# Kernel tuning notes

Measured on AMD Instinct MI355X. Metric: run time of the kernel, lower is better.

The kernel has to match this reference:

```python
import jax, jax.numpy as jnp
import numpy as np
from jax import lax

B, DIM, H, W = 32, 64, 1, 8192
HEADS = 8
EPS_LN = 1e-5
EPS_NORM = 1e-12


def setup_inputs() -> dict:
    key = jax.random.key(0)
    ks = jax.random.split(key, 20)
    g = lambda i, shape, s=0.05: jax.random.normal(ks[i], shape, jnp.float32) * s
    return dict(
        x=jax.random.normal(ks[0], (B, DIM, H, W), jnp.float32),
        qkv_w=g(1, (3 * DIM, DIM)), qkv_b=g(2, (3 * DIM,)),
        dw_w=g(3, (3 * DIM, 1, 3, 3)), dw_b=g(4, (3 * DIM,)),
        proj_w=g(5, (DIM, DIM)), proj_b=g(6, (DIM,)),
        temperature=jnp.ones((HEADS, 1, 1), jnp.float32),
        sp_w=g(7, (DIM,)), sp_b=g(8, (1,)),
        up_w=g(9, (3,)), up_b=g(10, (3,)),
        c2_w=g(11, (1, 1, 2)), c2_b=g(11, (1,)), ln2_w=jnp.ones((W,), jnp.float32), ln2_b=jnp.zeros((W,), jnp.float32),
        c4_w=g(12, (1, 1, 4)), c4_b=g(13, (1,)), ln4_w=jnp.ones((W,), jnp.float32), ln4_b=jnp.zeros((W,), jnp.float32),
        c6_w=g(14, (1, 1, 6)), c6_b=g(15, (1,)), ln6_w=jnp.ones((W,), jnp.float32), ln6_b=jnp.zeros((W,), jnp.float32),
        mp_w=g(16, (DIM,)), mp_b=g(17, (DIM,)),
    )


def _mtl(xs, cw, cb, lw, lb):
    """Multiscale_Temporal_Layer: conv1d 'same' -> LayerNorm(W) -> ELU -> mean pool. xs: (b,1,w)."""
    k = cw.shape[-1]
    tot = k - 1
    lo = tot // 2  # torch 'same': extra pad goes to the right
    y = lax.conv_general_dilated(xs, cw, (1,), [(lo, tot - lo)],
                                 dimension_numbers=('NCH', 'OIH', 'NCH'))
    y = y + cb[None, :, None]
    mu = jnp.mean(y, -1, keepdims=True)
    var = jnp.mean((y - mu) ** 2, -1, keepdims=True)
    y = (y - mu) / jnp.sqrt(var + EPS_LN) * lw + lb
    y = jax.nn.elu(y)
    return jnp.mean(y, -1, keepdims=True)  # (b,1,1)


def _forward(x, qkv_w, qkv_b, dw_w, dw_b, proj_w, proj_b, temperature,
             sp_w, sp_b, up_w, up_b,
             c2_w, c2_b, ln2_w, ln2_b,
             c4_w, c4_b, ln4_w, ln4_b,
             c6_w, c6_b, ln6_w, ln6_b,
             mp_w, mp_b):
    b, c, h, w = x.shape
    hd = c // HEADS  # per-head channel dim
    # 1x1 conv qkv, then depthwise 3x3 conv
    qkv = jnp.einsum('oc,bchw->bohw', qkv_w, x) + qkv_b[None, :, None, None]
    qkv = lax.conv_general_dilated(qkv, dw_w, (1, 1), [(1, 1), (1, 1)],
                                   dimension_numbers=('NCHW', 'OIHW', 'NCHW'),
                                   feature_group_count=3 * c)
    qkv = qkv + dw_b[None, :, None, None]
    q, k, v = jnp.split(qkv, 3, axis=1)
    # Multiscale_Temporal_Attention on v: v is (b,c,1,w)
    xseq = (jnp.einsum('c,bcw->bw', sp_w, v[:, :, 0, :]) + sp_b)[:, None, :]  # (b,1,w)
    up = up_w[None, :, None] * xseq + up_b[None, :, None]  # (b,3,w)
    xx, yy, zz = up[:, 0:1], up[:, 1:2], up[:, 2:3]
    mout = (_mtl(xx, c2_w, c2_b, ln2_w, ln2_b) * xx
            + _mtl(yy, c4_w, c4_b, ln4_w, ln4_b) * yy
            + _mtl(zz, c6_w, c6_b, ln6_w, ln6_b) * zz)  # (b,1,w)
    v = mp_w[None, :, None] * mout + mp_b[None, :, None]  # (b,c,w) via 1x1 conv broadcast
    # channel (transposed) attention over n = h*w tokens
    n = h * w
    q = q.reshape(b, HEADS, hd, n)
    k = k.reshape(b, HEADS, hd, n)
    v = v.reshape(b, HEADS, hd, n)
    q = q / jnp.maximum(jnp.linalg.norm(q, axis=-1, keepdims=True), EPS_NORM)
    k = k / jnp.maximum(jnp.linalg.norm(k, axis=-1, keepdims=True), EPS_NORM)
    attn = jnp.einsum('bhcn,bhdn->bhcd', q, k) * temperature  # (b,heads,hd,hd)
    attn = jax.nn.softmax(attn, axis=-1)
    out = jnp.einsum('bhcd,bhdn->bhcn', attn, v).reshape(b, c, h, w)
    out = jnp.einsum('oc,bchw->bohw', proj_w, out) + proj_b[None, :, None, None]
    return out  # dropouts are identity in eval mode


def reference(x, qkv_w, qkv_b, dw_w, dw_b, proj_w, proj_b, temperature,
              sp_w, sp_b, up_w, up_b,
              c2_w, c2_b, ln2_w, ln2_b,
              c4_w, c4_b, ln4_w, ln4_b,
              c6_w, c6_b, ln6_w, ln6_b,
              mp_w, mp_b):
    return _forward(x, qkv_w, qkv_b, dw_w, dw_b, proj_w, proj_b, temperature,
                    sp_w, sp_b, up_w, up_b,
                    c2_w, c2_b, ln2_w, ln2_b,
                    c4_w, c4_b, ln4_w, ln4_b,
                    c6_w, c6_b, ln6_w, ln6_b,
                    mp_w, mp_b)
```

## Files before the change

kernel.cpp:

```cpp
#include <hip/hip_runtime.h>
#include <hip/hip_bf16.h>
#include <math.h>

#define Wd 8192
#define Bd 32
#define Ttile 64

#define OFF_G    0
#define OFF_H    192
#define OFF_BASE 195
#define OFF_XSEQ 256
#define OFF_PART (256 + Bd*Wd)
#define OFF_S    (OFF_PART + Bd*128*640)
#define OFF_M    (OFF_S + Bd*640)
#define OFF_E    (OFF_M + 96)
#define OFF_F    (OFF_E + Bd*64)
#define OFF_FRAG (OFF_F + Bd*64)

typedef __attribute__((ext_vector_type(8))) short bf16x8;
typedef __attribute__((ext_vector_type(4))) float f32x4;

__device__ __forceinline__ unsigned short f2bf(float v) {
    return __builtin_bit_cast(unsigned short, __float2bfloat16(v));
}
__device__ __forceinline__ float bf2f(unsigned short h) {
    return __builtin_bit_cast(float, (unsigned)h << 16);
}
__device__ __forceinline__ void split2(float v0, float v1, unsigned& hw, unsigned& lw) {
    unsigned short h0 = f2bf(v0), h1 = f2bf(v1);
    unsigned short l0 = f2bf(v0 - bf2f(h0)), l1 = f2bf(v1 - bf2f(h1));
    hw = (unsigned)h0 | ((unsigned)h1 << 16);
    lw = (unsigned)l0 | ((unsigned)l1 << 16);
}
__device__ __forceinline__ unsigned pk2(float v0, float v1) {
    return (unsigned)f2bf(v0) | ((unsigned)f2bf(v1) << 16);
}

__global__ __launch_bounds__(256) void k0_setup(const float* __restrict__ qkv_w,
                         const float* __restrict__ qkv_b,
                         const float* __restrict__ dw_w, const float* __restrict__ dw_b,
                         const float* __restrict__ sp_w, const float* __restrict__ sp_b,
                         float* __restrict__ ws)
{
    int tid = threadIdx.x;
    if (tid < 192) {
        int j = tid >> 6, ch = tid & 63;
        float acc = 0.f;
        for (int c = 0; c < 64; c++)
            acc += sp_w[c] * dw_w[(128+c)*9 + 3 + j] * qkv_w[(128+c)*64 + ch];
        ws[OFF_G + j*64 + ch] = acc;
    } else if (tid < 195) {
        int j = tid - 192;
        float h = 0.f;
        for (int c = 0; c < 64; c++)
            h += sp_w[c] * dw_w[(128+c)*9 + 3 + j] * qkv_b[128+c];
        ws[OFF_H + j] = h;
    } else if (tid == 195) {
        float base = sp_b[0];
        for (int c = 0; c < 64; c++) base += sp_w[c] * dw_b[128+c];
        ws[OFF_BASE] = base;
    }
    __syncthreads();
    for (int it = tid; it < 36*64; it += 256) {
        int lane = it & 63;
        int cidx = it >> 6;
        int ver = cidx / 18;
        int rem = cidx - ver*18;
        int nt = rem >> 1, kb = rem & 1;
        int row = nt*16 + (lane & 15);
        int ks  = kb*32 + (lane >> 4)*8;
        unsigned short u[8];
        #pragma unroll
        for (int e = 0; e < 8; e++) {
            int k = ks + e;
            float v = 0.f;
            if (row < 128)      v = qkv_w[row*64 + k];
            else if (row < 131) v = ws[OFF_G + (row-128)*64 + k];
            unsigned short h = f2bf(v);
            if (ver == 0) u[e] = h;
            else          u[e] = f2bf(v - bf2f(h));
        }
        unsigned* dst = (unsigned*)(ws + OFF_FRAG) + (ver*1152 + (nt*2+kb)*64 + lane)*4;
        dst[0] = (unsigned)u[0] | ((unsigned)u[1] << 16);
        dst[1] = (unsigned)u[2] | ((unsigned)u[3] << 16);
        dst[2] = (unsigned)u[4] | ((unsigned)u[5] << 16);
        dst[3] = (unsigned)u[6] | ((unsigned)u[7] << 16);
    }
}

#define XT_HI 0
#define XT_LO 10752
#define QKH   21504
#define ZLDS  37888
#define SMEM_BYTES (37888 + 1024)

__global__ __launch_bounds__(256, 4) void k1_main(const float* __restrict__ x,
    const float* __restrict__ qkv_b, const float* __restrict__ dw_w,
    const float* __restrict__ dw_b, float* __restrict__ ws)
{
    __shared__ __align__(16) unsigned char smem[SMEM_BYTES];
    const int tid = threadIdx.x, lane = tid & 63, wv = tid >> 6;
    const int g = lane >> 4, lr = lane & 15;
    const int tile = blockIdx.x, b = blockIdx.y;
    const int w0 = tile * Ttile;
    const float* xb = x + (size_t)b * 64 * Wd;
    const bool safe = (tile != 0) && (tile != 127);

    for (int i = tid; i < 672; i += 256) {
        int j = i >> 5, chp = i & 31;
        int pos0 = w0 - 4 + 4*j;
        float4 a, c;
        if (safe || (unsigned)pos0 < (unsigned)Wd) {
            a = *(const float4*)(xb + (size_t)(2*chp)*Wd + pos0);
            c = *(const float4*)(xb + (size_t)(2*chp+1)*Wd + pos0);
        } else {
            a = (float4){0,0,0,0}; c = (float4){0,0,0,0};
        }
        #pragma unroll
        for (int e = 0; e < 4; e++) {
            int row = 4*j + e;
            float va = ((const float*)&a)[e], vc = ((const float*)&c)[e];
            unsigned hw, lw;
            split2(va, vc, hw, lw);
            int boff = row*128 + ((((chp>>2) ^ (row & 7)) << 4) | ((chp & 3) << 2));
            *(unsigned*)(smem + XT_HI + boff) = hw;
            *(unsigned*)(smem + XT_LO + boff) = lw;
        }
    }
    __syncthreads();

    f32x4 acc[3][5];
    #pragma unroll
    for (int i = 0; i < 3; i++)
        #pragma unroll
        for (int m = 0; m < 5; m++) acc[i][m] = (f32x4){0.f,0.f,0.f,0.f};
    const uint4* fragbase = (const uint4*)(ws + OFF_FRAG);

    #pragma unroll
    for (int kb = 0; kb < 2; kb++) {
        bf16x8 axh[5], axl[5];
        #pragma unroll
        for (int mt = 0; mt < 5; mt++) {
            int row = mt*16 + lr + 3;
            int gran = (kb*4 + g) ^ (row & 7);
            axh[mt] = *(const bf16x8*)(smem + XT_HI + row*128 + gran*16);
            axl[mt] = *(const bf16x8*)(smem + XT_LO + row*128 + gran*16);
        }
        #pragma unroll
        for (int nti = 0; nti < 3; nti++) {
            if (nti < 2 || wv == 0) {
                int nt = (nti == 2) ? 8 : (wv + nti*4);
                bf16x8 bh = __builtin_bit_cast(bf16x8, fragbase[(nt*2+kb)*64 + lane]);
                bf16x8 bl = __builtin_bit_cast(bf16x8, fragbase[1152 + (nt*2+kb)*64 + lane]);
                #pragma unroll
                for (int mt = 0; mt < 5; mt++) {
                    acc[nti][mt] = __builtin_amdgcn_mfma_f32_16x16x32_bf16(axh[mt], bh, acc[nti][mt], 0,0,0);
                    acc[nti][mt] = __builtin_amdgcn_mfma_f32_16x16x32_bf16(axl[mt], bh, acc[nti][mt], 0,0,0);
                    acc[nti][mt] = __builtin_amdgcn_mfma_f32_16x16x32_bf16(axh[mt], bl, acc[nti][mt], 0,0,0);
                }
            }
        }
    }

    float* zlds = (float*)(smem + ZLDS);
    #pragma unroll
    for (int nti = 0; nti < 3; nti++) {
        if (!(nti < 2 || wv == 0)) continue;
        int nt = (nti == 2) ? 8 : (wv + nti*4);
        int row = nt*16 + lr;
        if (nt == 8) {
            if (lr < 3) {
                #pragma unroll
                for (int mt = 0; mt < 5; mt++) {
                    float4 vz = { acc[2][mt][0], acc[2][mt][1], acc[2][mt][2], acc[2][mt][3] };
                    *(float4*)(zlds + lr*84 + mt*16 + g*4) = vz;
                }
            }
        } else {
            float bias = qkv_b[row];
            float tb = dw_b[row];
            float t0 = dw_w[row*9+3], t1 = dw_w[row*9+4], t2 = dw_w[row*9+5];
            float4 v[5];
            #pragma unroll
            for (int mt = 0; mt < 5; mt++) {
                #pragma unroll
                for (int r = 0; r < 4; r++) {
                    float val = acc[nti][mt][r] + bias;
                    if (!safe) {
                        int pos = w0 - 1 + mt*16 + g*4 + r;
                        if (pos < 0 || pos >= Wd) val = 0.f;
                    }
                    ((float*)&v[mt])[r] = val;
                }
            }
            int src = (lane + 16) & 63;
            #pragma unroll
            for (int mt = 0; mt < 4; mt++) {
                float a0 = __shfl(v[mt].x,   src), b0 = __shfl(v[mt+1].x, src);
                float a1 = __shfl(v[mt].y,   src), b1 = __shfl(v[mt+1].y, src);
                float in4 = (lane < 48) ? a0 : b0;
                float in5 = (lane < 48) ? a1 : b1;
                float o0 = tb + t0*v[mt].x + t1*v[mt].y + t2*v[mt].z;
                float o1 = tb + t0*v[mt].y + t1*v[mt].z + t2*v[mt].w;
                float o2 = tb + t0*v[mt].z + t1*v[mt].w + t2*in4;
                float o3 = tb + t0*v[mt].w + t1*in4     + t2*in5;
                uint2 hw;
                hw.x = pk2(o0, o1);
                hw.y = pk2(o2, o3);
                int gran = (2*mt + (g>>1)) ^ (row & 7);
                int boff = row*128 + (gran << 4) + ((g & 1) << 3);
                *(uint2*)(smem + QKH + boff) = hw;
            }
        }
    }

    if (tid < 64) {
        float a = ws[OFF_BASE];
        #pragma unroll
        for (int j = 0; j < 3; j++) {
            int wg = w0 + tid + j - 1;
            a += zlds[j*84 + tid + j];
            if (wg >= 0 && wg < Wd) a += ws[OFF_H + j];
        }
        ws[OFF_XSEQ + (size_t)b*Wd + w0 + tid] = a;
    }

    {
        const int rq = wv*16 + lr;
        const int rk = 64 + wv*16 + lr;
        f32x4 sqk = (f32x4){0,0,0,0}, sqq = (f32x4){0,0,0,0}, skk = (f32x4){0,0,0,0};
        #pragma unroll
        for (int kb = 0; kb < 2; kb++) {
            int gran = (kb*4 + g) ^ (lr & 7);
            bf16x8 qh = *(const bf16x8*)(smem + QKH + rq*128 + gran*16);
            bf16x8 kh = *(const bf16x8*)(smem + QKH + rk*128 + gran*16);
            sqk = __builtin_amdgcn_mfma_f32_16x16x32_bf16(qh, kh, sqk, 0,0,0);
            sqq = __builtin_amdgcn_mfma_f32_16x16x32_bf16(qh, qh, sqq, 0,0,0);
            skk = __builtin_amdgcn_mfma_f32_16x16x32_bf16(kh, kh, skk, 0,0,0);
        }
        float* pb = ws + OFF_PART + (size_t)(b*128 + tile)*640;
        int hh = lr >> 3, c2 = lr & 7;
        if (hh == (g >> 1)) {
            #pragma unroll
            for (int r = 0; r < 4; r++) {
                int c1 = (g & 1)*4 + r;
                pb[(2*wv + hh)*64 + c1*8 + c2] = sqk[r];
            }
        }
        if ((lr >> 2) == g) {
            int r = lr & 3;
            pb[512 + wv*16 + lr] = sqq[r];
            pb[576 + wv*16 + lr] = skk[r];
        }
    }
}

__device__ __forceinline__ float blk_reduce_256(float v, float* sc) {
    #pragma unroll
    for (int off = 32; off > 0; off >>= 1) v += __shfl_down(v, off, 64);
    __syncthreads();
    if ((threadIdx.x & 63) == 0) sc[threadIdx.x >> 6] = v;
    __syncthreads();
    return sc[0] + sc[1] + sc[2] + sc[3];
}

__global__ __launch_bounds__(256) void k23(const float* __restrict__ ws,
    const float* __restrict__ up_w, const float* __restrict__ up_b,
    const float* __restrict__ c2_w, const float* __restrict__ c2_b,
    const float* __restrict__ ln2_w, const float* __restrict__ ln2_b,
    const float* __restrict__ c4_w, const float* __restrict__ c4_b,
    const float* __restrict__ ln4_w, const float* __restrict__ ln4_b,
    const float* __restrict__ c6_w, const float* __restrict__ c6_b,
    const float* __restrict__ ln6_w, const float* __restrict__ ln6_b,
    float* __restrict__ wsS, float* __restrict__ wsM)
{
    __shared__ float ys[Wd];
    __shared__ float sc[4];
    int bx = blockIdx.x;
    if (bx < 32) {
        int b = bx;
        const float* part = ws + OFF_PART + (size_t)b*128*640;
        #pragma unroll
        for (int k = 0; k < 3; k++) {
            int idx = threadIdx.x + k*256;
            if (idx < 640) {
                float s0 = 0.f, s1 = 0.f, s2 = 0.f, s3 = 0.f;
                for (int t = 0; t < 128; t += 4) {
                    s0 += part[(size_t)(t  )*640 + idx];
                    s1 += part[(size_t)(t+1)*640 + idx];
                    s2 += part[(size_t)(t+2)*640 + idx];
                    s3 += part[(size_t)(t+3)*640 + idx];
                }
                wsS[b*640 + idx] = (s0 + s1) + (s2 + s3);
            }
        }
        return;
    }
    int t2 = bx - 32;
    int br = t2 / 32, b = t2 % 32;
    const float *cw, *lw, *lb; float cb; int K, lo;
    if (br == 0)      { cw = c2_w; cb = c2_b[0]; lw = ln2_w; lb = ln2_b; K = 2; lo = 0; }
    else if (br == 1) { cw = c4_w; cb = c4_b[0]; lw = ln4_w; lb = ln4_b; K = 4; lo = 1; }
    else              { cw = c6_w; cb = c6_b[0]; lw = ln6_w; lb = ln6_b; K = 6; lo = 2; }
    float uw = up_w[br], ub = up_b[br];
    const float* xr = ws + OFF_XSEQ + (size_t)b*Wd;

    float s = 0.f, s2 = 0.f;
    for (int w = threadIdx.x; w < Wd; w += 256) {
        float y = cb;
        for (int m = 0; m < K; m++) {
            int p = w + m - lo;
            if (p >= 0 && p < Wd) y += cw[m] * (uw*xr[p] + ub);
        }
        ys[w] = y; s += y; s2 += y*y;
    }
    float mu = blk_reduce_256(s, sc) * (1.f/Wd);
    __syncthreads();
    float Ey2 = blk_reduce_256(s2, sc) * (1.f/Wd);
    float var = fmaxf(Ey2 - mu*mu, 0.f);
    float inv = 1.f / sqrtf(var + 1e-5f);
    float se = 0.f;
    for (int w = threadIdx.x; w < Wd; w += 256) {
        float tt = (ys[w]-mu)*inv*lw[w] + lb[w];
        se += (tt > 0.f) ? tt : expm1f(tt);
    }
    float m = blk_reduce_256(se, sc) * (1.f/Wd);
    if (threadIdx.x == 0) wsM[b*3 + br] = m;
}

__global__ __launch_bounds__(256) void k45(const float* __restrict__ ws,
    const float* __restrict__ temperature,
    const float* __restrict__ mp_w, const float* __restrict__ mp_b,
    const float* __restrict__ up_w, const float* __restrict__ up_b,
    const float* __restrict__ proj_w, const float* __restrict__ proj_b,
    float* __restrict__ out)
{
    __shared__ float snk[64], sal[64], sbe[64], sE[64], sF[64];
    const int tid = threadIdx.x;
    const int chunk = blockIdx.x, b = blockIdx.y;
    const float* Sb = ws + OFF_S + b*640;
    float nq = 0.f;
    if (tid < 64) {
        nq = fmaxf(sqrtf(Sb[512 + tid]), 1e-12f);
        snk[tid] = fmaxf(sqrtf(Sb[576 + tid]), 1e-12f);
    }
    __syncthreads();
    if (tid < 64) {
        int h = tid >> 3;
        float temp = temperature[h];
        float lg[8], mx = -1e30f;
        #pragma unroll
        for (int d = 0; d < 8; d++) {
            lg[d] = Sb[8*tid + d] / (nq * snk[h*8 + d]) * temp;
            mx = fmaxf(mx, lg[d]);
        }
        float sum = 0.f;
        #pragma unroll
        for (int d = 0; d < 8; d++) { lg[d] = expf(lg[d] - mx); sum += lg[d]; }
        float a = 0.f, bb = 0.f;
        #pragma unroll
        for (int d = 0; d < 8; d++) {
            float at = lg[d] / sum;
            a  += at * mp_w[h*8 + d];
            bb += at * mp_b[h*8 + d];
        }
        sal[tid] = a; sbe[tid] = bb;
    }
    __syncthreads();
    if (tid < 64) {
        const float* wm = ws + OFF_M + b*3;
        float m2 = wm[0], m4 = wm[1], m6 = wm[2];
        float A = m2*up_w[0] + m4*up_w[1] + m6*up_w[2];
        float C = m2*up_b[0] + m4*up_b[1] + m6*up_b[2];
        float Pa = 0.f, Pb = 0.f;
        for (int c = 0; c < 64; c++) {
            float pw = proj_w[tid*64 + c];
            Pa += pw * sal[c];
            Pb += pw * sbe[c];
        }
        sE[tid] = A * Pa;
        sF[tid] = C * Pa + Pb + proj_b[tid];
    }
    __syncthreads();
    const float4* xs4 = (const float4*)(ws + OFF_XSEQ + (size_t)b*Wd);
    float4 xv = xs4[chunk*128 + (tid & 127)];
    int ohalf = tid >> 7;
    float4* ob = (float4*)out + (size_t)b*64*2048 + chunk*128 + (tid & 127);
    #pragma unroll 8
    for (int oo = 0; oo < 32; oo++) {
        int o = ohalf*32 + oo;
        float e = sE[o], f = sF[o];
        float4 r = { e*xv.x + f, e*xv.y + f, e*xv.z + f, e*xv.w + f };
        ob[(size_t)o*2048] = r;
    }
}

extern "C" void kernel_launch(void* const* d_in, const int* in_sizes, int n_in,
                              void* d_out, int out_size, void* d_ws, size_t ws_size,
                              hipStream_t stream) {
    const float* x      = (const float*)d_in[0];
    const float* qkv_w  = (const float*)d_in[1];
    const float* qkv_b  = (const float*)d_in[2];
    const float* dw_w   = (const float*)d_in[3];
    const float* dw_b   = (const float*)d_in[4];
    const float* proj_w = (const float*)d_in[5];
    const float* proj_b = (const float*)d_in[6];
    const float* temperature = (const float*)d_in[7];
    const float* sp_w   = (const float*)d_in[8];
    const float* sp_b   = (const float*)d_in[9];
    const float* up_w   = (const float*)d_in[10];
    const float* up_b   = (const float*)d_in[11];
    const float* c2_w   = (const float*)d_in[12];
    const float* c2_b   = (const float*)d_in[13];
    const float* ln2_w  = (const float*)d_in[14];
    const float* ln2_b  = (const float*)d_in[15];
    const float* c4_w   = (const float*)d_in[16];
    const float* c4_b   = (const float*)d_in[17];
    const float* ln4_w  = (const float*)d_in[18];
    const float* ln4_b  = (const float*)d_in[19];
    const float* c6_w   = (const float*)d_in[20];
    const float* c6_b   = (const float*)d_in[21];
    const float* ln6_w  = (const float*)d_in[22];
    const float* ln6_b  = (const float*)d_in[23];
    const float* mp_w   = (const float*)d_in[24];
    const float* mp_b   = (const float*)d_in[25];
    float* ws  = (float*)d_ws;
    float* out = (float*)d_out;

    k0_setup<<<1, 256, 0, stream>>>(qkv_w, qkv_b, dw_w, dw_b, sp_w, sp_b, ws);
    k1_main<<<dim3(128, 32), 256, 0, stream>>>(x, qkv_b, dw_w, dw_b, ws);
    k23<<<128, 256, 0, stream>>>(ws, up_w, up_b,
        c2_w, c2_b, ln2_w, ln2_b, c4_w, c4_b, ln4_w, ln4_b, c6_w, c6_b, ln6_w, ln6_b,
        ws + OFF_S, ws + OFF_M);
    k45<<<dim3(16, 32), 256, 0, stream>>>(ws, temperature, mp_w, mp_b,
        up_w, up_b, proj_w, proj_b, out);
}
```

Measured before the change: 126.2 us.

## Compute attention Gram from shifted input autocorrelations instead of materializing q/k

Replaces the per-tile q/k projection plus depthwise conv plus Gram accumulation with a kernel that computes raw input lag-0/±1/±2 autocorrelation matrices of x in bf16 via MFMA, plus per-row sums. A new kernel then combines these with qkv and depthwise weights to reconstruct q·k, q·q and k·k algebraically, including boundary corrections. This cuts MFMA work and the split hi/lo bf16 triple product, but x is now rounded to single bf16, which risks precision loss. The sequence projection is computed inside the same pass with double-buffered LDS staging.

```diff
diff --git a/kernel.cpp b/kernel.cpp
--- a/kernel.cpp
+++ b/kernel.cpp
@@ -4,18 +4,16 @@
 
 #define Wd 8192
 #define Bd 32
-#define Ttile 64
 
 #define OFF_G    0
 #define OFF_H    192
 #define OFF_BASE 195
 #define OFF_XSEQ 256
-#define OFF_PART (256 + Bd*Wd)
-#define OFF_S    (OFF_PART + Bd*128*640)
-#define OFF_M    (OFF_S + Bd*640)
-#define OFF_E    (OFF_M + 96)
-#define OFF_F    (OFF_E + Bd*64)
-#define OFF_FRAG (OFF_F + Bd*64)
+#define OFF_SXP  (OFF_XSEQ + Bd*Wd)
+#define OFF_RX   (OFF_SXP + Bd*8*64)
+#define OFF_T    (OFF_RX + Bd*8*12288)
+#define OFF_VEC  (OFF_T + Bd*3*1152)
+#define OFF_WM   (OFF_VEC + Bd*640)
 
 typedef __attribute__((ext_vector_type(8))) short bf16x8;
 typedef __attribute__((ext_vector_type(4))) float f32x4;
@@ -25,15 +23,6 @@
 }
 __device__ __forceinline__ float bf2f(unsigned short h) {
     return __builtin_bit_cast(float, (unsigned)h << 16);
-}
-__device__ __forceinline__ void split2(float v0, float v1, unsigned& hw, unsigned& lw) {
-    unsigned short h0 = f2bf(v0), h1 = f2bf(v1);
-    unsigned short l0 = f2bf(v0 - bf2f(h0)), l1 = f2bf(v1 - bf2f(h1));
-    hw = (unsigned)h0 | ((unsigned)h1 << 16);
-    lw = (unsigned)l0 | ((unsigned)l1 << 16);
-}
-__device__ __forceinline__ unsigned pk2(float v0, float v1) {
-    return (unsigned)f2bf(v0) | ((unsigned)f2bf(v1) << 16);
 }
 
 __global__ __launch_bounds__(256) void k0_setup(const float* __restrict__ qkv_w,
@@ -42,219 +31,183 @@
                          const float* __restrict__ sp_w, const float* __restrict__ sp_b,
                          float* __restrict__ ws)
 {
+    __shared__ float sw[64*64];
+    __shared__ float sdw[192];
+    __shared__ float ssp[64], sqb[64], sdb[64];
     int tid = threadIdx.x;
+    for (int i = tid; i < 4096; i += 256) sw[i] = qkv_w[128*64 + i];
+    if (tid < 192) { int c = tid/3, j = tid - 3*c; sdw[tid] = dw_w[(128+c)*9 + 3 + j]; }
+    if (tid < 64)  { ssp[tid] = sp_w[tid]; sqb[tid] = qkv_b[128+tid]; sdb[tid] = dw_b[128+tid]; }
+    __syncthreads();
     if (tid < 192) {
         int j = tid >> 6, ch = tid & 63;
         float acc = 0.f;
+        #pragma unroll 8
         for (int c = 0; c < 64; c++)
-            acc += sp_w[c] * dw_w[(128+c)*9 + 3 + j] * qkv_w[(128+c)*64 + ch];
+            acc += ssp[c] * sdw[c*3+j] * sw[c*64 + ch];
         ws[OFF_G + j*64 + ch] = acc;
     } else if (tid < 195) {
         int j = tid - 192;
         float h = 0.f;
+        #pragma unroll 8
         for (int c = 0; c < 64; c++)
-            h += sp_w[c] * dw_w[(128+c)*9 + 3 + j] * qkv_b[128+c];
+            h += ssp[c] * sdw[c*3+j] * sqb[c];
         ws[OFF_H + j] = h;
     } else if (tid == 195) {
         float base = sp_b[0];
-        for (int c = 0; c < 64; c++) base += sp_w[c] * dw_b[128+c];
+        #pragma unroll 8
+        for (int c = 0; c < 64; c++) base += ssp[c] * sdb[c];
         ws[OFF_BASE] = base;
     }
-    __syncthreads();
-    for (int it = tid; it < 36*64; it += 256) {
-        int lane = it & 63;
-        int cidx = it >> 6;
-        int ver = cidx / 18;
-        int rem = cidx - ver*18;
-        int nt = rem >> 1, kb = rem & 1;
-        int row = nt*16 + (lane & 15);
-        int ks  = kb*32 + (lane >> 4)*8;
-        unsigned short u[8];
-        #pragma unroll
-        for (int e = 0; e < 8; e++) {
-            int k = ks + e;
-            float v = 0.f;
-            if (row < 128)      v = qkv_w[row*64 + k];
-            else if (row < 131) v = ws[OFF_G + (row-128)*64 + k];
-            unsigned short h = f2bf(v);
-            if (ver == 0) u[e] = h;
-            else          u[e] = f2bf(v - bf2f(h));
-        }
-        unsigned* dst = (unsigned*)(ws + OFF_FRAG) + (ver*1152 + (nt*2+kb)*64 + lane)*4;
-        dst[0] = (unsigned)u[0] | ((unsigned)u[1] << 16);
-        dst[1] = (unsigned)u[2] | ((unsigned)u[3] << 16);
-        dst[2] = (unsigned)u[4] | ((unsigned)u[5] << 16);
-        dst[3] = (unsigned)u[6] | ((unsigned)u[7] << 16);
-    }
-}
-
-#define XT_HI 0
-#define XT_LO 10752
-#define QKH   21504
-#define ZLDS  37888
-#define SMEM_BYTES (37888 + 1024)
-
-__global__ __launch_bounds__(256, 4) void k1_main(const float* __restrict__ x,
-    const float* __restrict__ qkv_b, const float* __restrict__ dw_w,
-    const float* __restrict__ dw_b, float* __restrict__ ws)
+}
+
+#define XSTR 152
+#define XBYTES (64*XSTR*2)
+
+__device__ __forceinline__ void loadpf(const float* __restrict__ xr, int wstart,
+                                       int q, float4 pf[9]) {
+    #pragma unroll
+    for (int m = 0; m < 9; m++) {
+        int gp = wstart - 8 + 36*q + 4*m;
+        if (gp >= 0 && gp < Wd) pf[m] = *(const float4*)(xr + gp);
+        else pf[m] = (float4){0.f,0.f,0.f,0.f};
+    }
+}
+__device__ __forceinline__ float writepf(unsigned char* buf, int row, int q,
+                                         const float4 pf[9]) {
+    float ss = 0.f;
+    #pragma unroll
+    for (int m = 0; m < 9; m++) {
+        int col0 = 36*q + 4*m;
+        unsigned short h0 = f2bf(pf[m].x), h1 = f2bf(pf[m].y),
+                       h2 = f2bf(pf[m].z), h3 = f2bf(pf[m].w);
+        uint2 wv;
+        wv.x = (unsigned)h0 | ((unsigned)h1 << 16);
+        wv.y = (unsigned)h2 | ((unsigned)h3 << 16);
+        *(uint2*)(buf + row*304 + col0*2) = wv;
+        if (col0 >= 8 && col0 < 136)
+            ss += (bf2f(h0) + bf2f(h1)) + (bf2f(h2) + bf2f(h3));
+    }
+    return ss;
+}
+
+__global__ __launch_bounds__(256) void kR(const float* __restrict__ x,
+                                          float* __restrict__ ws)
 {
-    __shared__ __align__(16) unsigned char smem[SMEM_BYTES];
+    __shared__ __align__(16) unsigned char xb0[XBYTES];
+    __shared__ __align__(16) unsigned char xb1[XBYTES];
+    __shared__ float4 Gl[64];
+    __shared__ float phib[3][132];
+    __shared__ float sxb[64][4];
+
     const int tid = threadIdx.x, lane = tid & 63, wv = tid >> 6;
     const int g = lane >> 4, lr = lane & 15;
-    const int tile = blockIdx.x, b = blockIdx.y;
-    const int w0 = tile * Ttile;
-    const float* xb = x + (size_t)b * 64 * Wd;
-    const bool safe = (tile != 0) && (tile != 127);
-
-    for (int i = tid; i < 672; i += 256) {
-        int j = i >> 5, chp = i & 31;
-        int pos0 = w0 - 4 + 4*j;
-        float4 a, c;
-        if (safe || (unsigned)pos0 < (unsigned)Wd) {
-            a = *(const float4*)(xb + (size_t)(2*chp)*Wd + pos0);
-            c = *(const float4*)(xb + (size_t)(2*chp+1)*Wd + pos0);
-        } else {
-            a = (float4){0,0,0,0}; c = (float4){0,0,0,0};
-        }
-        #pragma unroll
-        for (int e = 0; e < 4; e++) {
-            int row = 4*j + e;
-            float va = ((const float*)&a)[e], vc = ((const float*)&c)[e];
-            unsigned hw, lw;
-            split2(va, vc, hw, lw);
-            int boff = row*128 + ((((chp>>2) ^ (row & 7)) << 4) | ((chp & 3) << 2));
-            *(unsigned*)(smem + XT_HI + boff) = hw;
-            *(unsigned*)(smem + XT_LO + boff) = lw;
-        }
-    }
-    __syncthreads();
-
-    f32x4 acc[3][5];
+    const int chunk = blockIdx.x, b = blockIdx.y;
+    const int w0 = chunk << 10;
+    const int row = tid & 63, q = tid >> 6;
+    const float* xr = x + ((size_t)b*64 + row)*Wd;
+
+    if (tid < 64) Gl[tid] = (float4){ws[OFF_G+tid], ws[OFF_G+64+tid], ws[OFF_G+128+tid], 0.f};
+    const float Hs0 = ws[OFF_H], Hs1 = ws[OFF_H+1], Hs2 = ws[OFF_H+2];
+    const float base_ = ws[OFF_BASE];
+
+    f32x4 a0[4], a1[4], a2[4];
     #pragma unroll
-    for (int i = 0; i < 3; i++)
-        #pragma unroll
-        for (int m = 0; m < 5; m++) acc[i][m] = (f32x4){0.f,0.f,0.f,0.f};
-    const uint4* fragbase = (const uint4*)(ws + OFF_FRAG);
-
+    for (int ct = 0; ct < 4; ct++) {
+        a0[ct] = (f32x4){0,0,0,0}; a1[ct] = (f32x4){0,0,0,0}; a2[ct] = (f32x4){0,0,0,0};
+    }
+    float ssum = 0.f;
+    float4 pf[9];
+
+    loadpf(xr, w0, q, pf);
+    ssum += writepf(xb0, row, q, pf);
+    __syncthreads();
+
+    for (int st = 0; st < 8; ++st) {
+        const int p0 = w0 + (st << 7);
+        unsigned char* bufc = (st & 1) ? xb1 : xb0;
+        unsigned char* bufn = (st & 1) ? xb0 : xb1;
+
+        if (st < 7) loadpf(xr, p0 + 128, q, pf);
+
+        #pragma unroll
+        for (int k = 0; k < 4; k++) {
+            const unsigned char* ap = bufc + (16*wv + lr)*304 + 16 + 64*k + 16*g;
+            bf16x8 A = *(const bf16x8*)ap;
+            #pragma unroll
+            for (int ct = 0; ct < 4; ct++) {
+                const unsigned char* bp = bufc + (16*ct + lr)*304 + 16 + 64*k + 16*g;
+                uint4 u = *(const uint4*)bp;
+                unsigned u4 = *(const unsigned*)(bp + 16);
+                uint4 v1 = { (u.x>>16)|(u.y<<16), (u.y>>16)|(u.z<<16),
+                             (u.z>>16)|(u.w<<16), (u.w>>16)|(u4<<16) };
+                uint4 v2 = { u.y, u.z, u.w, u4 };
+                a0[ct] = __builtin_amdgcn_mfma_f32_16x16x32_bf16(A, __builtin_bit_cast(bf16x8,u),  a0[ct],0,0,0);
+                a1[ct] = __builtin_amdgcn_mfma_f32_16x16x32_bf16(A, __builtin_bit_cast(bf16x8,v1), a1[ct],0,0,0);
+                a2[ct] = __builtin_amdgcn_mfma_f32_16x16x32_bf16(A, __builtin_bit_cast(bf16x8,v2), a2[ct],0,0,0);
+            }
+        }
+        if (tid < 130) {
+            const unsigned short* xs = (const unsigned short*)bufc;
+            float f0=0.f, f1=0.f, f2=0.f;
+            int colw = 7 + tid;
+            #pragma unroll 8
+            for (int c = 0; c < 64; c++) {
+                float xv = bf2f(xs[c*XSTR + colw]);
+                float4 gv = Gl[c];
+                f0 += gv.x*xv; f1 += gv.y*xv; f2 += gv.z*xv;
+            }
+            phib[0][tid]=f0; phib[1][tid]=f1; phib[2][tid]=f2;
+        }
+        __syncthreads();
+        if (tid < 128) {
+            int w = p0 + tid;
+            float v = base_ + Hs0 + Hs1 + Hs2
+                    + phib[0][tid] + phib[1][tid+1] + phib[2][tid+2];
+            if (w == 0) v -= Hs0;
+            if (w == Wd-1) v -= Hs2;
+            ws[OFF_XSEQ + (size_t)b*Wd + w] = v;
+        }
+        if (st < 7) ssum += writepf(bufn, row, q, pf);
+        __syncthreads();
+    }
+
+    {
+        float* pb = ws + OFF_RX + (size_t)(b*8 + chunk)*12288;
+        #pragma unroll
+        for (int ct = 0; ct < 4; ct++) {
+            #pragma unroll
+            for (int r = 0; r < 4; r++) {
+                int c = 16*wv + 4*g + r, cc = 16*ct + lr;
+                pb[         c*64 + cc] = a0[ct][r];
+                pb[4096  +  c*64 + cc] = a1[ct][r];
+                pb[8192  +  c*64 + cc] = a2[ct][r];
+            }
+        }
+    }
+    sxb[row][q] = ssum;
+    __syncthreads();
+    if (tid < 64)
+        ws[OFF_SXP + (size_t)(b*8 + chunk)*64 + tid] =
+            (sxb[tid][0] + sxb[tid][1]) + (sxb[tid][2] + sxb[tid][3]);
+}
+
+#define KF_SW 0
+#define KF_RX (128*68*4)
+#define KF_NT (KF_RX + 64*68*4)
+#define KF_SXR (KF_NT + 64*68*4)
+#define KF_XC (KF_SXR + 64*4)
+#define KF_BYTES (KF_XC + 256*4)
+
+__device__ __forceinline__ float dot64p(const float* a, const float* b) {
+    float s0=0.f,s1=0.f,s2=0.f,s3=0.f;
     #pragma unroll
-    for (int kb = 0; kb < 2; kb++) {
-        bf16x8 axh[5], axl[5];
-        #pragma unroll
-        for (int mt = 0; mt < 5; mt++) {
-            int row = mt*16 + lr + 3;
-            int gran = (kb*4 + g) ^ (row & 7);
-            axh[mt] = *(const bf16x8*)(smem + XT_HI + row*128 + gran*16);
-            axl[mt] = *(const bf16x8*)(smem + XT_LO + row*128 + gran*16);
-        }
-        #pragma unroll
-        for (int nti = 0; nti < 3; nti++) {
-            if (nti < 2 || wv == 0) {
-                int nt = (nti == 2) ? 8 : (wv + nti*4);
-                bf16x8 bh = __builtin_bit_cast(bf16x8, fragbase[(nt*2+kb)*64 + lane]);
-                bf16x8 bl = __builtin_bit_cast(bf16x8, fragbase[1152 + (nt*2+kb)*64 + lane]);
-                #pragma unroll
-                for (int mt = 0; mt < 5; mt++) {
-                    acc[nti][mt] = __builtin_amdgcn_mfma_f32_16x16x32_bf16(axh[mt], bh, acc[nti][mt], 0,0,0);
-                    acc[nti][mt] = __builtin_amdgcn_mfma_f32_16x16x32_bf16(axl[mt], bh, acc[nti][mt], 0,0,0);
-                    acc[nti][mt] = __builtin_amdgcn_mfma_f32_16x16x32_bf16(axh[mt], bl, acc[nti][mt], 0,0,0);
-                }
-            }
-        }
-    }
-
-    float* zlds = (float*)(smem + ZLDS);
-    #pragma unroll
-    for (int nti = 0; nti < 3; nti++) {
-        if (!(nti < 2 || wv == 0)) continue;
-        int nt = (nti == 2) ? 8 : (wv + nti*4);
-        int row = nt*16 + lr;
-        if (nt == 8) {
-            if (lr < 3) {
-                #pragma unroll
-                for (int mt = 0; mt < 5; mt++) {
-                    float4 vz = { acc[2][mt][0], acc[2][mt][1], acc[2][mt][2], acc[2][mt][3] };
-                    *(float4*)(zlds + lr*84 + mt*16 + g*4) = vz;
-                }
-            }
-        } else {
-            float bias = qkv_b[row];
-            float tb = dw_b[row];
-            float t0 = dw_w[row*9+3], t1 = dw_w[row*9+4], t2 = dw_w[row*9+5];
-            float4 v[5];
-            #pragma unroll
-            for (int mt = 0; mt < 5; mt++) {
-                #pragma unroll
-                for (int r = 0; r < 4; r++) {
-                    float val = acc[nti][mt][r] + bias;
-                    if (!safe) {
-                        int pos = w0 - 1 + mt*16 + g*4 + r;
-                        if (pos < 0 || pos >= Wd) val = 0.f;
-                    }
-                    ((float*)&v[mt])[r] = val;
-                }
-            }
-            int src = (lane + 16) & 63;
-            #pragma unroll
-            for (int mt = 0; mt < 4; mt++) {
-                float a0 = __shfl(v[mt].x,   src), b0 = __shfl(v[mt+1].x, src);
-                float a1 = __shfl(v[mt].y,   src), b1 = __shfl(v[mt+1].y, src);
-                float in4 = (lane < 48) ? a0 : b0;
-                float in5 = (lane < 48) ? a1 : b1;
-                float o0 = tb + t0*v[mt].x + t1*v[mt].y + t2*v[mt].z;
-                float o1 = tb + t0*v[mt].y + t1*v[mt].z + t2*v[mt].w;
-                float o2 = tb + t0*v[mt].z + t1*v[mt].w + t2*in4;
-                float o3 = tb + t0*v[mt].w + t1*in4     + t2*in5;
-                uint2 hw;
-                hw.x = pk2(o0, o1);
-                hw.y = pk2(o2, o3);
-                int gran = (2*mt + (g>>1)) ^ (row & 7);
-                int boff = row*128 + (gran << 4) + ((g & 1) << 3);
-                *(uint2*)(smem + QKH + boff) = hw;
-            }
-        }
-    }
-
-    if (tid < 64) {
-        float a = ws[OFF_BASE];
-        #pragma unroll
-        for (int j = 0; j < 3; j++) {
-            int wg = w0 + tid + j - 1;
-            a += zlds[j*84 + tid + j];
-            if (wg >= 0 && wg < Wd) a += ws[OFF_H + j];
-        }
-        ws[OFF_XSEQ + (size_t)b*Wd + w0 + tid] = a;
-    }
-
-    {
-        const int rq = wv*16 + lr;
-        const int rk = 64 + wv*16 + lr;
-        f32x4 sqk = (f32x4){0,0,0,0}, sqq = (f32x4){0,0,0,0}, skk = (f32x4){0,0,0,0};
-        #pragma unroll
-        for (int kb = 0; kb < 2; kb++) {
-            int gran = (kb*4 + g) ^ (lr & 7);
-            bf16x8 qh = *(const bf16x8*)(smem + QKH + rq*128 + gran*16);
-            bf16x8 kh = *(const bf16x8*)(smem + QKH + rk*128 + gran*16);
-            sqk = __builtin_amdgcn_mfma_f32_16x16x32_bf16(qh, kh, sqk, 0,0,0);
-            sqq = __builtin_amdgcn_mfma_f32_16x16x32_bf16(qh, qh, sqq, 0,0,0);
-            skk = __builtin_amdgcn_mfma_f32_16x16x32_bf16(kh, kh, skk, 0,0,0);
-        }
-        float* pb = ws + OFF_PART + (size_t)(b*128 + tile)*640;
-        int hh = lr >> 3, c2 = lr & 7;
-        if (hh == (g >> 1)) {
-            #pragma unroll
-            for (int r = 0; r < 4; r++) {
-                int c1 = (g & 1)*4 + r;
-                pb[(2*wv + hh)*64 + c1*8 + c2] = sqk[r];
-            }
-        }
-        if ((lr >> 2) == g) {
-            int r = lr & 3;
-            pb[512 + wv*16 + lr] = sqq[r];
-            pb[576 + wv*16 + lr] = skk[r];
-        }
-    }
-}
-
+    for (int k = 0; k < 64; k += 4) {
+        float4 av = *(const float4*)(a+k), bv = *(const float4*)(b+k);
+        s0 += av.x*bv.x; s1 += av.y*bv.y; s2 += av.z*bv.z; s3 += av.w*bv.w;
+    }
+    return (s0+s1)+(s2+s3);
+}
 __device__ __forceinline__ float blk_reduce_256(float v, float* sc) {
     #pragma unroll
     for (int off = 32; off > 0; off >>= 1) v += __shfl_down(v, off, 64);
@@ -264,7 +217,8 @@
     return sc[0] + sc[1] + sc[2] + sc[3];
 }
 
-__global__ __launch_bounds__(256) void k23(const float* __restrict__ ws,
+__global__ __launch_bounds__(256) void kF(const float* __restrict__ x,
+    const float* __restrict__ qkv_w,
     const float* __restrict__ up_w, const float* __restrict__ up_b,
     const float* __restrict__ c2_w, const float* __restrict__ c2_b,
     const float* __restrict__ ln2_w, const float* __restrict__ ln2_b,
@@ -272,32 +226,128 @@
     const float* __restrict__ ln4_w, const float* __restrict__ ln4_b,
     const float* __restrict__ c6_w, const float* __restrict__ c6_b,
     const float* __restrict__ ln6_w, const float* __restrict__ ln6_b,
-    float* __restrict__ wsS, float* __restrict__ wsM)
+    float* __restrict__ ws)
 {
-    __shared__ float ys[Wd];
+    __shared__ __align__(16) unsigned char sm[KF_BYTES];
     __shared__ float sc[4];
-    int bx = blockIdx.x;
-    if (bx < 32) {
-        int b = bx;
-        const float* part = ws + OFF_PART + (size_t)b*128*640;
-        #pragma unroll
-        for (int k = 0; k < 3; k++) {
-            int idx = threadIdx.x + k*256;
-            if (idx < 640) {
-                float s0 = 0.f, s1 = 0.f, s2 = 0.f, s3 = 0.f;
-                for (int t = 0; t < 128; t += 4) {
-                    s0 += part[(size_t)(t  )*640 + idx];
-                    s1 += part[(size_t)(t+1)*640 + idx];
-                    s2 += part[(size_t)(t+2)*640 + idx];
-                    s3 += part[(size_t)(t+3)*640 + idx];
-                }
-                wsS[b*640 + idx] = (s0 + s1) + (s2 + s3);
-            }
-        }
+    const int tid = threadIdx.x, bx = blockIdx.x;
+
+    if (bx < 96) {
+        const int bb = bx / 3, d = bx - 3*bb;
+        float* sW  = (float*)(sm + KF_SW);
+        float* sRx = (float*)(sm + KF_RX);
+        float* sNT = (float*)(sm + KF_NT);
+        float* sxr = (float*)(sm + KF_SXR);
+        float* xcol = (float*)(sm + KF_XC);
+
+        #pragma unroll
+        for (int k = 0; k < 8; k++) {
+            int i4 = tid + 256*k;
+            float4 v = ((const float4*)qkv_w)[i4];
+            int r = i4 >> 4, c = (i4 & 15) << 2;
+            *(float4*)(sW + r*68 + c) = v;
+        }
+        const float* rxp = ws + OFF_RX + (size_t)bb*8*12288 + d*4096;
+        #pragma unroll
+        for (int k = 0; k < 16; k++) {
+            int idx = tid + 256*k;
+            float s = 0.f;
+            #pragma unroll
+            for (int ch = 0; ch < 8; ch++) s += rxp[(size_t)ch*12288 + idx];
+            sRx[(idx>>6)*68 + (idx&63)] = s;
+        }
+        if (d == 0) {
+            if (tid < 64) {
+                float s = 0.f;
+                #pragma unroll
+                for (int ch = 0; ch < 8; ch++) s += ws[OFF_SXP + (size_t)(bb*8+ch)*64 + tid];
+                sxr[tid] = s;
+            }
+            {
+                int c = tid & 63, v = tid >> 6;
+                int colv = (v == 0) ? 0 : (v == 1) ? 1 : (v == 2) ? (Wd-2) : (Wd-1);
+                xcol[v*64 + c] = x[((size_t)bb*64 + c)*Wd + colv];
+            }
+        }
+        __syncthreads();
+        if (d == 0 && tid < 128) {
+            int r = tid;
+            float Xi=0.f,x0=0.f,x1=0.f,xm2=0.f,xm1=0.f;
+            #pragma unroll 8
+            for (int c = 0; c < 64; c++) {
+                float w = sW[r*68+c];
+                Xi += w*sxr[c]; x0 += w*xcol[c]; x1 += w*xcol[64+c];
+                xm2 += w*xcol[128+c]; xm1 += w*xcol[192+c];
+            }
+            float* vp = ws + OFF_VEC + bb*640;
+            vp[r] = Xi; vp[128+r] = x0; vp[256+r] = x1; vp[384+r] = xm2; vp[512+r] = xm1;
+        }
+        {
+            int ro = tid >> 4, co = tid & 15;
+            float acc[4][4] = {};
+            for (int k = 0; k < 64; k += 4) {
+                float4 av[4], bv[4];
+                #pragma unroll
+                for (int i = 0; i < 4; i++) av[i] = *(const float4*)(sRx + (4*ro+i)*68 + k);
+                #pragma unroll
+                for (int j = 0; j < 4; j++) bv[j] = *(const float4*)(sW + (64+4*co+j)*68 + k);
+                #pragma unroll
+                for (int i = 0; i < 4; i++)
+                    #pragma unroll
+                    for (int j = 0; j < 4; j++)
+                        acc[i][j] += av[i].x*bv[j].x + av[i].y*bv[j].y
+                                   + av[i].z*bv[j].z + av[i].w*bv[j].w;
+            }
+            __syncthreads();
+            #pragma unroll
+            for (int i = 0; i < 4; i++)
+                #pragma unroll
+                for (int j = 0; j < 4; j++)
+                    sNT[(4*co+j)*68 + 4*ro+i] = acc[i][j];
+        }
+        __syncthreads();
+        float* Tp = ws + OFF_T + (size_t)(bb*3 + d)*1152;
+        for (int e = tid; e < 512; e += 256) {
+            int t = e >> 3, u = ((e>>6)<<3) + (e&7);
+            Tp[e] = dot64p(sW + t*68, sNT + u*68);
+        }
+        if (tid < 64) Tp[1088 + tid] = dot64p(sW + (64+tid)*68, sNT + tid*68);
+        __syncthreads();
+        {
+            int ro = tid >> 4, co = tid & 15;
+            float acc[4][4] = {};
+            for (int k = 0; k < 64; k += 4) {
+                float4 av[4], bv[4];
+                #pragma unroll
+                for (int i = 0; i < 4; i++) av[i] = *(const float4*)(sRx + (4*ro+i)*68 + k);
+                #pragma unroll
+                for (int j = 0; j < 4; j++) bv[j] = *(const float4*)(sW + (4*co+j)*68 + k);
+                #pragma unroll
+                for (int i = 0; i < 4; i++)
+                    #pragma unroll
+                    for (int j = 0; j < 4; j++)
+                        acc[i][j] += av[i].x*bv[j].x + av[i].y*bv[j].y
+                                   + av[i].z*bv[j].z + av[i].w*bv[j].w;
+            }
+            __syncthreads();
+            #pragma unroll
+            for (int i = 0; i < 4; i++)
+                #pragma unroll
+                for (int j = 0; j < 4; j++)
+                    sNT[(4*co+j)*68 + 4*ro+i] = acc[i][j];
+        }
+        __syncthreads();
+        for (int e = tid; e < 512; e += 256) {
+            int t = e >> 3, u = ((e>>6)<<3) + (e&7);
+            Tp[512 + e] = dot64p(sW + (64+u)*68, sNT + t*68);
+        }
+        if (tid < 64) Tp[1024 + tid] = dot64p(sW + tid*68, sNT + tid*68);
         return;
     }
-    int t2 = bx - 32;
-    int br = t2 / 32, b = t2 % 32;
+
+    int t2 = bx - 96;
+    int br = t2 >> 5, b = t2 & 31;
+    float* ys = (float*)sm;
     const float *cw, *lw, *lb; float cb; int K, lo;
     if (br == 0)      { cw = c2_w; cb = c2_b[0]; lw = ln2_w; lb = ln2_b; K = 2; lo = 0; }
     else if (br == 1) { cw = c4_w; cb = c4_b[0]; lw = ln4_w; lb = ln4_b; K = 4; lo = 1; }
@@ -306,7 +356,7 @@
     const float* xr = ws + OFF_XSEQ + (size_t)b*Wd;
 
     float s = 0.f, s2 = 0.f;
-    for (int w = threadIdx.x; w < Wd; w += 256) {
+    for (int w = tid; w < Wd; w += 256) {
         float y = cb;
         for (int m = 0; m < K; m++) {
             int p = w + m - lo;
@@ -320,29 +370,101 @@
     float var = fmaxf(Ey2 - mu*mu, 0.f);
     float inv = 1.f / sqrtf(var + 1e-5f);
     float se = 0.f;
-    for (int w = threadIdx.x; w < Wd; w += 256) {
+    for (int w = tid; w < Wd; w += 256) {
         float tt = (ys[w]-mu)*inv*lw[w] + lb[w];
         se += (tt > 0.f) ? tt : expm1f(tt);
     }
     float m = blk_reduce_256(se, sc) * (1.f/Wd);
-    if (threadIdx.x == 0) wsM[b*3 + br] = m;
-}
-
-__global__ __launch_bounds__(256) void k45(const float* __restrict__ ws,
-    const float* __restrict__ temperature,
+    if (tid == 0) ws[OFF_WM + b*3 + br] = m;
+}
+
+__global__ __launch_bounds__(256) void k5_out(const float* __restrict__ ws,
+    const float* __restrict__ qkv_b, const float* __restrict__ dw_w,
+    const float* __restrict__ dw_b, const float* __restrict__ temperature,
     const float* __restrict__ mp_w, const float* __restrict__ mp_b,
     const float* __restrict__ up_w, const float* __restrict__ up_b,
     const float* __restrict__ proj_w, const float* __restrict__ proj_b,
     float* __restrict__ out)
 {
+    __shared__ float sT3[3][1152];
+    __shared__ float vec[5][128];
+    __shared__ float qb_[128], tb_[128], tp_[128][3];
+    __shared__ float Sq[512], dgq[64], dgk[64];
     __shared__ float snk[64], sal[64], sbe[64], sE[64], sF[64];
+    __shared__ float red[64][8];
     const int tid = threadIdx.x;
     const int chunk = blockIdx.x, b = blockIdx.y;
-    const float* Sb = ws + OFF_S + b*640;
+
+    for (int i = tid; i < 3456; i += 256) ((float*)sT3)[i] = ws[OFF_T + (size_t)b*3456 + i];
+    for (int i = tid; i < 640; i += 256) ((float*)vec)[i] = ws[OFF_VEC + b*640 + i];
+    if (tid < 128) {
+        qb_[tid] = qkv_b[tid]; tb_[tid] = dw_b[tid];
+        tp_[tid][0] = dw_w[tid*9+3]; tp_[tid][1] = dw_w[tid*9+4]; tp_[tid][2] = dw_w[tid*9+5];
+    }
+    __syncthreads();
+
+    for (int ee = tid; ee < 640; ee += 256) {
+        int r, s; float Tpv[3], Tmv[3];
+        if (ee < 512) {
+            r = ee >> 3; s = 64 + ((ee>>6)<<3) + (ee&7);
+            #pragma unroll
+            for (int d = 0; d < 3; d++) { Tpv[d] = sT3[d][ee]; Tmv[d] = sT3[d][512+ee]; }
+        } else if (ee < 576) {
+            r = s = ee - 512;
+            #pragma unroll
+            for (int d = 0; d < 3; d++) { Tpv[d] = Tmv[d] = sT3[d][1024 + r]; }
+        } else {
+            int u = ee - 576; r = s = 64 + u;
+            #pragma unroll
+            for (int d = 0; d < 3; d++) { Tpv[d] = Tmv[d] = sT3[d][1088 + u]; }
+        }
+        float Xr = vec[0][r], Xs = vec[0][s];
+        float x0r = vec[1][r], x0s = vec[1][s];
+        float x1r = vec[2][r], x1s = vec[2][s];
+        float xm2r = vec[3][r], xm2s = vec[3][s];
+        float xm1r = vec[4][r], xm1s = vec[4][s];
+        float qr = qb_[r], qs = qb_[s];
+        float C5[5];
+        #pragma unroll
+        for (int dd = 0; dd < 3; dd++) {
+            float head_s = (dd>=1 ? x0s : 0.f) + (dd>=2 ? x1s : 0.f);
+            float tail_r = (dd>=1 ? xm1r : 0.f) + (dd>=2 ? xm2r : 0.f);
+            C5[2+dd] = Tpv[dd] + qr*(Xs - head_s) + qs*(Xr - tail_r) + (8192.f - dd)*qr*qs;
+            float head_r = (dd>=1 ? x0r : 0.f) + (dd>=2 ? x1r : 0.f);
+            float tail_s = (dd>=1 ? xm1s : 0.f) + (dd>=2 ? xm2s : 0.f);
+            C5[2-dd] = Tmv[dd] + qs*(Xr - head_r) + qr*(Xs - tail_s) + (8192.f - dd)*qr*qs;
+        }
+        float y0r = x0r + qr, y0s = x0s + qs;
+        float ym1r = xm1r + qr, ym1s = xm1s + qs;
+        float Yr = Xr + 8192.f*qr, Ys = Xs + 8192.f*qs;
+        float tbr = tb_[r], tbs = tb_[s];
+        float G = 8192.f * tbr * tbs;
+        float sumr = 0.f, sums = 0.f;
+        #pragma unroll
+        for (int i = 0; i < 3; i++) {
+            sumr += tp_[r][i] * (Yr - (i==0 ? ym1r : 0.f) - (i==2 ? y0r : 0.f));
+            sums += tp_[s][i] * (Ys - (i==0 ? ym1s : 0.f) - (i==2 ? y0s : 0.f));
+        }
+        G += tbr * sums + tbs * sumr;
+        #pragma unroll
+        for (int i = 0; i < 3; i++)
+            #pragma unroll
+            for (int j = 0; j < 3; j++) {
+                float P = C5[2 + j - i];
+                if (i == 2 && j == 2) P -= y0r * y0s;
+                if (i == 0 && j == 0) P -= ym1r * ym1s;
+                G += tp_[r][i] * tp_[s][j] * P;
+            }
+        if (ee < 512) Sq[ee] = G;
+        else if (ee < 576) dgq[ee-512] = G;
+        else dgk[ee-576] = G;
+    }
+    __syncthreads();
+
     float nq = 0.f;
     if (tid < 64) {
-        nq = fmaxf(sqrtf(Sb[512 + tid]), 1e-12f);
-        snk[tid] = fmaxf(sqrtf(Sb[576 + tid]), 1e-12f);
+        nq = fmaxf(sqrtf(fmaxf(dgq[tid], 0.f)), 1e-12f);
+        snk[tid] = fmaxf(sqrtf(fmaxf(dgk[tid], 0.f)), 1e-12f);
     }
     __syncthreads();
     if (tid < 64) {
@@ -351,47 +473,54 @@
         float lg[8], mx = -1e30f;
         #pragma unroll
         for (int d = 0; d < 8; d++) {
-            lg[d] = Sb[8*tid + d] / (nq * snk[h*8 + d]) * temp;
+            lg[d] = Sq[tid*8 + d] / (nq * snk[h*8 + d]) * temp;
             mx = fmaxf(mx, lg[d]);
         }
         float sum = 0.f;
         #pragma unroll
         for (int d = 0; d < 8; d++) { lg[d] = expf(lg[d] - mx); sum += lg[d]; }
-        float a = 0.f, bb = 0.f;
+        float a = 0.f, bb2 = 0.f;
         #pragma unroll
         for (int d = 0; d < 8; d++) {
             float at = lg[d] / sum;
-            a  += at * mp_w[h*8 + d];
-            bb += at * mp_b[h*8 + d];
-        }
-        sal[tid] = a; sbe[tid] = bb;
-    }
-    __syncthreads();
-    if (tid < 64) {
-        const float* wm = ws + OFF_M + b*3;
-        float m2 = wm[0], m4 = wm[1], m6 = wm[2];
-        float A = m2*up_w[0] + m4*up_w[1] + m6*up_w[2];
-        float C = m2*up_b[0] + m4*up_b[1] + m6*up_b[2];
-        float Pa = 0.f, Pb = 0.f;
-        for (int c = 0; c < 64; c++) {
-            float pw = proj_w[tid*64 + c];
-            Pa += pw * sal[c];
-            Pb += pw * sbe[c];
-        }
-        sE[tid] = A * Pa;
-        sF[tid] = C * Pa + Pb + proj_b[tid];
+            a   += at * mp_w[h*8 + d];
+            bb2 += at * mp_b[h*8 + d];
+        }
+        sal[tid] = a; sbe[tid] = bb2;
+    }
+    __syncthreads();
+    {
+        float m2 = ws[OFF_WM + b*3], m4 = ws[OFF_WM + b*3 + 1], m6 = ws[OFF_WM + b*3 + 2];
+        float A_ = m2*up_w[0] + m4*up_w[1] + m6*up_w[2];
+        float C_ = m2*up_b[0] + m4*up_b[1] + m6*up_b[2];
+        int o = tid & 63, q = tid >> 6;
+        float pa = 0.f, pb2 = 0.f;
+        #pragma unroll
+        for (int k = 0; k < 16; k++) {
+            int c = 16*q + k;
+            float pw = proj_w[o*64 + c];
+            pa += pw * sal[c]; pb2 += pw * sbe[c];
+        }
+        red[o][q] = pa; red[o][4+q] = pb2;
+        __syncthreads();
+        if (tid < 64) {
+            float Pa = (red[tid][0]+red[tid][1]) + (red[tid][2]+red[tid][3]);
+            float Pb = (red[tid][4]+red[tid][5]) + (red[tid][6]+red[tid][7]);
+            sE[tid] = A_ * Pa;
+            sF[tid] = C_ * Pa + Pb + proj_b[tid];
+        }
     }
     __syncthreads();
     const float4* xs4 = (const float4*)(ws + OFF_XSEQ + (size_t)b*Wd);
     float4 xv = xs4[chunk*128 + (tid & 127)];
-    int ohalf = tid >> 7;
+    int oh = tid >> 7;
     float4* ob = (float4*)out + (size_t)b*64*2048 + chunk*128 + (tid & 127);
     #pragma unroll 8
     for (int oo = 0; oo < 32; oo++) {
-        int o = ohalf*32 + oo;
+        int o = oh*32 + oo;
         float e = sE[o], f = sF[o];
-        float4 r = { e*xv.x + f, e*xv.y + f, e*xv.z + f, e*xv.w + f };
-        ob[(size_t)o*2048] = r;
+        float4 rr = { e*xv.x + f, e*xv.y + f, e*xv.z + f, e*xv.w + f };
+        ob[(size_t)o*2048] = rr;
     }
 }
 
@@ -428,10 +557,10 @@
     float* out = (float*)d_out;
 
     k0_setup<<<1, 256, 0, stream>>>(qkv_w, qkv_b, dw_w, dw_b, sp_w, sp_b, ws);
-    k1_main<<<dim3(128, 32), 256, 0, stream>>>(x, qkv_b, dw_w, dw_b, ws);
-    k23<<<128, 256, 0, stream>>>(ws, up_w, up_b,
+    kR<<<dim3(8, 32), 256, 0, stream>>>(x, ws);
+    kF<<<192, 256, 0, stream>>>(x, qkv_w, up_w, up_b,
         c2_w, c2_b, ln2_w, ln2_b, c4_w, c4_b, ln4_w, ln4_b, c6_w, c6_b, ln6_w, ln6_b,
-        ws + OFF_S, ws + OFF_M);
-    k45<<<dim3(16, 32), 256, 0, stream>>>(ws, temperature, mp_w, mp_b,
-        up_w, up_b, proj_w, proj_b, out);
-}
+        ws);
+    k5_out<<<dim3(16, 32), 256, 0, stream>>>(ws, qkv_b, dw_w, dw_b, temperature,
+        mp_w, mp_b, up_w, up_b, proj_w, proj_b, out);
+}
```

New measurement: 129.1 us. +2.3%, slower.
